# Optimization experiments

Hardware: AMD Instinct MI355X
Metric: run time of the kernel (lower is better)

The kernel has to match this reference:

```python
import jax, jax.numpy as jnp
import numpy as np

D_IN, D_OUT, SEQ, BATCH = 768, 768, 4096, 4

def setup_inputs() -> dict:
    key = jax.random.key(0)
    k0, k1, k2, k3 = jax.random.split(key, 4)
    s = 1.0 / np.sqrt(D_IN)
    return {
        "input_batch": jax.random.normal(k0, (BATCH, SEQ, D_IN), dtype=jnp.float32),
        "Wq": jax.random.uniform(k1, (D_OUT, D_IN), jnp.float32, -s, s),
        "Wk": jax.random.uniform(k2, (D_OUT, D_IN), jnp.float32, -s, s),
        "Wv": jax.random.uniform(k3, (D_OUT, D_IN), jnp.float32, -s, s),
    }

def reference(input_batch, Wq, Wk, Wv):
    B, N, d_in = input_batch.shape
    q = jnp.einsum('bnd,od->bno', input_batch, Wq)  # [B,N,d_out]
    k = jnp.einsum('bnd,od->bno', input_batch, Wk)
    v = jnp.einsum('bnd,od->bno', input_batch, Wv)
    scores = jnp.einsum('bqo,bko->bqk', q, k)  # [B,N,N]
    causal = jnp.tril(jnp.ones((N, N), dtype=bool))
    scores = jnp.where(causal, scores, -jnp.inf)
    # note: original scales by d_in (input embedding dim), not d_out
    weights = jax.nn.softmax(scores / jnp.sqrt(jnp.asarray(d_in, scores.dtype)), axis=-1)
    return jnp.einsum('bqk,bko->bqo', weights, v)
```

## Files before the change

kernel.cpp:

```cpp
#include <hip/hip_runtime.h>
#include <hip/hip_bf16.h>
#include <stdint.h>

#define NSEQ 4096
#define DDIM 768
#define NB   4
#define NTRI 528
#define BLKE 16384

typedef short short8 __attribute__((ext_vector_type(8)));
typedef float f32x16 __attribute__((ext_vector_type(16)));

__device__ __forceinline__ unsigned short f2bf(float f) {
    unsigned int u = __float_as_uint(f);
    u += 0x7fffu + ((u >> 16) & 1u);
    return (unsigned short)(u >> 16);
}
__device__ __forceinline__ float bf2f(unsigned short h) {
    return __uint_as_float(((unsigned int)h) << 16);
}
__device__ __forceinline__ short8 cvt8(const float* __restrict__ p) {
    float4 x = *(const float4*)p;
    float4 y = *(const float4*)(p + 4);
    union { short8 s; __hip_bfloat162 h[4]; } u;
    u.h[0] = __float22bfloat162_rn(make_float2(x.x, x.y));
    u.h[1] = __float22bfloat162_rn(make_float2(x.z, x.w));
    u.h[2] = __float22bfloat162_rn(make_float2(y.x, y.y));
    u.h[3] = __float22bfloat162_rn(make_float2(y.z, y.w));
    return u.s;
}

typedef const __attribute__((address_space(1))) unsigned int ga_u32;
typedef __attribute__((address_space(3))) unsigned int ls_u32;
__device__ __forceinline__ void gload_lds16(const void* g, void* l) {
    __builtin_amdgcn_global_load_lds((ga_u32*)(uintptr_t)g, (ls_u32*)(uintptr_t)l, 16, 0, 0);
}

__device__ __forceinline__ void stage_tile(const unsigned short* gbase, int stride,
                                           unsigned short* lds, int tid) {
    const int lane = tid & 63, wv = tid >> 6;
    const int r8  = lane >> 3;
    const int csw = ((lane & 7) ^ r8) * 8;
    const int cl  = (lane & 7) * 8;
#pragma unroll
    for (int t = 0; t < 4; ++t) {
        const int row = wv * 32 + t * 8 + r8;
        gload_lds16(gbase + (size_t)row * stride + csw, lds + row * 64 + cl);
    }
}

__device__ __forceinline__ void mma_tiles(const unsigned short* As, const unsigned short* Bs,
                                          f32x16 acc[2][2], int wm, int wn, int lane) {
    const int r32 = lane & 31;
    const int hi  = lane >> 5;
    const int sw  = lane & 7;
#pragma unroll
    for (int c = 0; c < 4; ++c) {
        const int chunk = ((c * 2 + hi) ^ sw) * 8;
        short8 af[2], bg[2];
#pragma unroll
        for (int mt = 0; mt < 2; ++mt)
            af[mt] = *(const short8*)(As + (wm * 64 + mt * 32 + r32) * 64 + chunk);
#pragma unroll
        for (int nt = 0; nt < 2; ++nt)
            bg[nt] = *(const short8*)(Bs + (wn * 64 + nt * 32 + r32) * 64 + chunk);
#pragma unroll
        for (int mt = 0; mt < 2; ++mt)
#pragma unroll
            for (int nt = 0; nt < 2; ++nt)
                acc[mt][nt] = __builtin_amdgcn_mfma_f32_32x32x16_bf16(af[mt], bg[nt], acc[mt][nt], 0, 0, 0);
    }
}

__device__ __forceinline__ int crow(int reg, int hi) {
    return (reg & 3) + 8 * (reg >> 2) + 4 * hi;
}

__global__ __launch_bounds__(256)
void convert_kernel(const float* __restrict__ X, const float* __restrict__ Wq,
                    const float* __restrict__ Wk, const float* __restrict__ Wv,
                    unsigned short* __restrict__ Xb, unsigned short* __restrict__ Wb,
                    unsigned int* __restrict__ counter)
{
    const int bid = blockIdx.x;
    if (bid == 0 && threadIdx.x == 0) *counter = 0u;
    const float* src; unsigned short* dst; size_t off;
    if (bid < 6144) { src = X; dst = Xb; off = (size_t)bid * 2048; }
    else {
        const int wbid = bid - 6144;
        const int wi = wbid / 288;
        src = (wi == 0) ? Wq : ((wi == 1) ? Wk : Wv);
        dst = Wb + (size_t)wi * (DDIM * DDIM);
        off = (size_t)(wbid - wi * 288) * 2048;
    }
    const size_t i = off + (size_t)threadIdx.x * 8;
    *(short8*)(dst + i) = cvt8(src + i);
}

__global__ __launch_bounds__(256)
void qkv_gemm(const unsigned short* __restrict__ Xb, const unsigned short* __restrict__ Wb,
              unsigned short* __restrict__ Qb, unsigned short* __restrict__ Kb,
              unsigned short* __restrict__ Vtb)
{
    const int tid = threadIdx.x, lane = tid & 63, wv = tid >> 6;
    const int r32 = lane & 31, hi = lane >> 5, wm = wv >> 1, wn = wv & 1;
    const int m0 = blockIdx.x * 128, n0 = blockIdx.y * 128, widx = blockIdx.z;
    const unsigned short* A = Xb + (size_t)m0 * DDIM;
    const unsigned short* B = Wb + (size_t)widx * (DDIM * DDIM) + (size_t)n0 * DDIM;

    __shared__ __align__(16) unsigned short As[128 * 64];
    __shared__ __align__(16) unsigned short Bs[128 * 64];

    f32x16 acc[2][2] = {};

    for (int kt = 0; kt < 12; ++kt) {
        stage_tile(A + kt * 64, DDIM, As, tid);
        stage_tile(B + kt * 64, DDIM, Bs, tid);
        __syncthreads();
        mma_tiles(As, Bs, acc, wm, wn, lane);
        __syncthreads();
    }

    const int m_base = m0 + wm * 64, o_base = n0 + wn * 64;
    if (widx < 2) {
        unsigned short* dst = (widx == 0) ? Qb : Kb;
#pragma unroll
        for (int mt = 0; mt < 2; ++mt)
#pragma unroll
            for (int nt = 0; nt < 2; ++nt)
#pragma unroll
                for (int reg = 0; reg < 16; ++reg)
                    dst[(size_t)(m_base + mt * 32 + crow(reg, hi)) * DDIM +
                        (o_base + nt * 32 + r32)] = f2bf(acc[mt][nt][reg]);
    } else {
        const int bb = m0 >> 12;
        const int n_seq0 = (m0 & (NSEQ - 1)) + wm * 64;
#pragma unroll
        for (int mt = 0; mt < 2; ++mt)
#pragma unroll
            for (int nt = 0; nt < 2; ++nt) {
                const int o = o_base + nt * 32 + r32;
#pragma unroll
                for (int b4 = 0; b4 < 4; ++b4) {
                    ushort4 pk;
                    pk.x = f2bf(acc[mt][nt][b4 * 4 + 0]);
                    pk.y = f2bf(acc[mt][nt][b4 * 4 + 1]);
                    pk.z = f2bf(acc[mt][nt][b4 * 4 + 2]);
                    pk.w = f2bf(acc[mt][nt][b4 * 4 + 3]);
                    const int n = n_seq0 + mt * 32 + b4 * 8 + hi * 4;
                    *(ushort4*)(Vtb + ((size_t)(bb * DDIM + o)) * NSEQ + n) = pk;
                }
            }
    }
}

__global__ __launch_bounds__(256)
void gemm_s(const unsigned short* __restrict__ Qb, const unsigned short* __restrict__ Kb,
            unsigned short* __restrict__ Sbuf)
{
    const int tid = threadIdx.x, lane = tid & 63, wv = tid >> 6;
    const int r32 = lane & 31, hi = lane >> 5, wm = wv >> 1, wn = wv & 1;
    const int idx = blockIdx.x, bb = blockIdx.y;
    int qb = (int)((sqrtf(8.f * idx + 1.f) - 1.f) * 0.5f);
    while ((qb + 1) * (qb + 2) / 2 <= idx) ++qb;
    while (qb * (qb + 1) / 2 > idx) --qb;
    const int kb = idx - qb * (qb + 1) / 2;

    const unsigned short* A = Qb + ((size_t)bb * NSEQ + qb * 128) * DDIM;
    const unsigned short* B = Kb + ((size_t)bb * NSEQ + kb * 128) * DDIM;

    __shared__ __align__(16) unsigned short As[128 * 64];
    __shared__ __align__(16) unsigned short Bs[128 * 64];

    f32x16 acc[2][2] = {};

    for (int kt = 0; kt < 12; ++kt) {
        stage_tile(A + kt * 64, DDIM, As, tid);
        stage_tile(B + kt * 64, DDIM, Bs, tid);
        __syncthreads();
        mma_tiles(As, Bs, acc, wm, wn, lane);
        __syncthreads();
    }

    unsigned short* Sblk = Sbuf + ((size_t)(bb * NTRI + idx)) * BLKE;
    const bool diag = (qb == kb);
#pragma unroll
    for (int mt = 0; mt < 2; ++mt)
#pragma unroll
        for (int nt = 0; nt < 2; ++nt)
#pragma unroll
            for (int reg = 0; reg < 16; ++reg) {
                const int row = wm * 64 + mt * 32 + crow(reg, hi);
                const int col = wn * 64 + nt * 32 + r32;
                unsigned short v = (diag && col > row) ? (unsigned short)0xFF80
                                                       : f2bf(acc[mt][nt][reg]);
                Sblk[row * 128 + col] = v;
            }
}

__global__ __launch_bounds__(256)
void softmax_kernel(unsigned short* __restrict__ S)
{
    const float c2 = 0.05205877475f;
    const int row = blockIdx.x * 4 + (threadIdx.x >> 6);
    const int lane = threadIdx.x & 63;
    const int bb = row >> 12, q = row & (NSEQ - 1);
    const int qb = q >> 7, ql = q & 127, nb = qb + 1;
    const size_t base = ((size_t)(bb * NTRI + qb * (qb + 1) / 2)) * BLKE + (size_t)ql * 128;
    const int g = lane >> 4, c = (lane & 15) * 8;

    const short NEGINF = (short)0xFF80;
    short8 regs[8];
#pragma unroll
    for (int it = 0; it < 8; ++it) {
        const int kb = it * 4 + g;
        if (kb < nb) {
            regs[it] = *(const short8*)(S + base + (size_t)kb * BLKE + c);
        } else {
            short8 v;
#pragma unroll
            for (int j = 0; j < 8; ++j) v[j] = NEGINF;
            regs[it] = v;
        }
    }

    float mx = -1e30f;
#pragma unroll
    for (int it = 0; it < 8; ++it)
#pragma unroll
        for (int j = 0; j < 8; ++j) mx = fmaxf(mx, bf2f((unsigned short)regs[it][j]));
#pragma unroll
    for (int s = 1; s < 64; s <<= 1) mx = fmaxf(mx, __shfl_xor(mx, s));

    float sum = 0.f;
#pragma unroll
    for (int it = 0; it < 8; ++it)
#pragma unroll
        for (int j = 0; j < 8; ++j)
            sum += exp2f((bf2f((unsigned short)regs[it][j]) - mx) * c2);
#pragma unroll
    for (int s = 1; s < 64; s <<= 1) sum += __shfl_xor(sum, s);
    const float inv = 1.0f / sum;

#pragma unroll
    for (int it = 0; it < 8; ++it) {
        const int kb = it * 4 + g;
        if (kb < nb) {
            short8 o;
#pragma unroll
            for (int j = 0; j < 8; ++j)
                o[j] = (short)f2bf(exp2f((bf2f((unsigned short)regs[it][j]) - mx) * c2) * inv);
            *(short8*)(S + base + (size_t)kb * BLKE + c) = o;
        }
    }
}

__global__ __launch_bounds__(256)
void gemm_pv(const unsigned short* __restrict__ P, const unsigned short* __restrict__ Vt,
             float* __restrict__ Out, unsigned int* __restrict__ counter)
{
    const int tid = threadIdx.x, lane = tid & 63, wv = tid >> 6;
    const int r32 = lane & 31, hi = lane >> 5, wm = wv >> 1, wn = wv & 1;

    __shared__ __align__(16) unsigned short As[128 * 64];
    __shared__ __align__(16) unsigned short Bs[128 * 64];
    __shared__ unsigned int item_s;

    for (;;) {
        if (tid == 0) item_s = atomicAdd(counter, 1u);
        __syncthreads();
        const unsigned int item = item_s;
        if (item >= 768u) return;

        const int t = (int)(item / 24u);
        const int qb = 31 - t;
        const int rem = (int)(item - (unsigned)t * 24u);
        const int bb = rem / 6, ob = rem % 6;
        const size_t triq = (size_t)qb * (qb + 1) / 2;
        const unsigned short* Pbat = P + (size_t)bb * NTRI * BLKE;
        const unsigned short* Bbase = Vt + ((size_t)(bb * DDIM + ob * 128)) * NSEQ;
        const int niter = (qb + 1) * 2;

        f32x16 acc[2][2] = {};

        for (int it = 0; it < niter; ++it) {
            const int k0 = it * 64;
            const int kblk = k0 >> 7, cb = k0 & 64;
            stage_tile(Pbat + (triq + kblk) * BLKE + cb, 128, As, tid);
            stage_tile(Bbase + k0, NSEQ, Bs, tid);
            __syncthreads();
            mma_tiles(As, Bs, acc, wm, wn, lane);
            __syncthreads();
        }

        const int q_base = qb * 128 + wm * 64;
        const int o_base = ob * 128 + wn * 64;
#pragma unroll
        for (int mt = 0; mt < 2; ++mt)
#pragma unroll
            for (int nt = 0; nt < 2; ++nt)
#pragma unroll
                for (int reg = 0; reg < 16; ++reg) {
                    const int q = q_base + mt * 32 + crow(reg, hi);
                    Out[((size_t)(bb * NSEQ + q)) * DDIM + (o_base + nt * 32 + r32)] =
                        acc[mt][nt][reg];
                }
    }
}

extern "C" void kernel_launch(void* const* d_in, const int* in_sizes, int n_in,
                              void* d_out, int out_size, void* d_ws, size_t ws_size,
                              hipStream_t stream)
{
    const float* X  = (const float*)d_in[0];
    const float* Wq = (const float*)d_in[1];
    const float* Wk = (const float*)d_in[2];
    const float* Wv = (const float*)d_in[3];
    float* Out = (float*)d_out;

    const size_t E = (size_t)NB * NSEQ * DDIM;
    char* ws = (char*)d_ws;
    unsigned short* Qb  = (unsigned short*)ws;
    unsigned short* Kb  = Qb + E;
    unsigned short* Vtb = Kb + E;
    unsigned short* Sbuf = Vtb + E;
    unsigned short* Xb  = Sbuf;
    unsigned short* Wb  = Xb + E;
    unsigned int* counter =
        (unsigned int*)(ws + 3 * E * 2 + (size_t)NB * NTRI * BLKE * 2);

    convert_kernel<<<7008, 256, 0, stream>>>(X, Wq, Wk, Wv, Xb, Wb, counter);
    qkv_gemm<<<dim3(128, 6, 3), 256, 0, stream>>>(Xb, Wb, Qb, Kb, Vtb);
    gemm_s<<<dim3(528, NB), 256, 0, stream>>>(Qb, Kb, Sbuf);
    softmax_kernel<<<4096, 256, 0, stream>>>(Sbuf);
    gemm_pv<<<512, 256, 0, stream>>>(Sbuf, Vtb, Out, counter);
}
```

Measured before the change: 381.4 us.

## Fuse softmax into score GEMM epilogue and defer normalization to PV GEMM

The separate softmax kernel is removed. The score GEMM epilogue now writes unnormalized exp2 values as bf16 and atomically accumulates per-row sums into a new L buffer, which the convert kernel zeroes. The PV GEMM scales each output row by the reciprocal of its row sum. This saves a full read and write pass over the score buffer and one kernel launch. The cost is a float atomic per row per block, and exponentials are taken without subtracting the row max, so large scores could overflow for inputs with a wider range than these.

```diff
diff --git a/kernel.cpp b/kernel.cpp
--- a/kernel.cpp
+++ b/kernel.cpp
@@ -80,10 +80,15 @@
 void convert_kernel(const float* __restrict__ X, const float* __restrict__ Wq,
                     const float* __restrict__ Wk, const float* __restrict__ Wv,
                     unsigned short* __restrict__ Xb, unsigned short* __restrict__ Wb,
-                    unsigned int* __restrict__ counter)
+                    float* __restrict__ L, unsigned int* __restrict__ counter)
 {
     const int bid = blockIdx.x;
     if (bid == 0 && threadIdx.x == 0) *counter = 0u;
+    if (bid >= 7008) {
+        const int idx = (bid - 7008) * 1024 + threadIdx.x * 4;
+        *(float4*)(L + idx) = make_float4(0.f, 0.f, 0.f, 0.f);
+        return;
+    }
     const float* src; unsigned short* dst; size_t off;
     if (bid < 6144) { src = X; dst = Xb; off = (size_t)bid * 2048; }
     else {
@@ -156,8 +161,9 @@
 
 __global__ __launch_bounds__(256)
 void gemm_s(const unsigned short* __restrict__ Qb, const unsigned short* __restrict__ Kb,
-            unsigned short* __restrict__ Sbuf)
-{
+            unsigned short* __restrict__ Sbuf, float* __restrict__ L)
+{
+    const float c2 = 0.05205877475f;
     const int tid = threadIdx.x, lane = tid & 63, wv = tid >> 6;
     const int r32 = lane & 31, hi = lane >> 5, wm = wv >> 1, wn = wv & 1;
     const int idx = blockIdx.x, bb = blockIdx.y;
@@ -183,87 +189,42 @@
     }
 
     unsigned short* Sblk = Sbuf + ((size_t)(bb * NTRI + idx)) * BLKE;
+    float* Lrow = L + (size_t)bb * NSEQ + qb * 128;
     const bool diag = (qb == kb);
 #pragma unroll
     for (int mt = 0; mt < 2; ++mt)
 #pragma unroll
-        for (int nt = 0; nt < 2; ++nt)
-#pragma unroll
-            for (int reg = 0; reg < 16; ++reg) {
-                const int row = wm * 64 + mt * 32 + crow(reg, hi);
+        for (int reg = 0; reg < 16; ++reg) {
+            const int row = wm * 64 + mt * 32 + crow(reg, hi);
+            float vsum = 0.f;
+#pragma unroll
+            for (int nt = 0; nt < 2; ++nt) {
                 const int col = wn * 64 + nt * 32 + r32;
-                unsigned short v = (diag && col > row) ? (unsigned short)0xFF80
-                                                       : f2bf(acc[mt][nt][reg]);
-                Sblk[row * 128 + col] = v;
+                float e = (diag && col > row) ? 0.f : exp2f(acc[mt][nt][reg] * c2);
+                const unsigned short pb = f2bf(e);
+                Sblk[row * 128 + col] = pb;
+                vsum += bf2f(pb);
             }
-}
-
-__global__ __launch_bounds__(256)
-void softmax_kernel(unsigned short* __restrict__ S)
-{
-    const float c2 = 0.05205877475f;
-    const int row = blockIdx.x * 4 + (threadIdx.x >> 6);
-    const int lane = threadIdx.x & 63;
-    const int bb = row >> 12, q = row & (NSEQ - 1);
-    const int qb = q >> 7, ql = q & 127, nb = qb + 1;
-    const size_t base = ((size_t)(bb * NTRI + qb * (qb + 1) / 2)) * BLKE + (size_t)ql * 128;
-    const int g = lane >> 4, c = (lane & 15) * 8;
-
-    const short NEGINF = (short)0xFF80;
-    short8 regs[8];
-#pragma unroll
-    for (int it = 0; it < 8; ++it) {
-        const int kb = it * 4 + g;
-        if (kb < nb) {
-            regs[it] = *(const short8*)(S + base + (size_t)kb * BLKE + c);
-        } else {
-            short8 v;
-#pragma unroll
-            for (int j = 0; j < 8; ++j) v[j] = NEGINF;
-            regs[it] = v;
+            vsum += __shfl_xor(vsum, 1);
+            vsum += __shfl_xor(vsum, 2);
+            vsum += __shfl_xor(vsum, 4);
+            vsum += __shfl_xor(vsum, 8);
+            vsum += __shfl_xor(vsum, 16);
+            if (r32 == 0) atomicAdd(&Lrow[row], vsum);
         }
-    }
-
-    float mx = -1e30f;
-#pragma unroll
-    for (int it = 0; it < 8; ++it)
-#pragma unroll
-        for (int j = 0; j < 8; ++j) mx = fmaxf(mx, bf2f((unsigned short)regs[it][j]));
-#pragma unroll
-    for (int s = 1; s < 64; s <<= 1) mx = fmaxf(mx, __shfl_xor(mx, s));
-
-    float sum = 0.f;
-#pragma unroll
-    for (int it = 0; it < 8; ++it)
-#pragma unroll
-        for (int j = 0; j < 8; ++j)
-            sum += exp2f((bf2f((unsigned short)regs[it][j]) - mx) * c2);
-#pragma unroll
-    for (int s = 1; s < 64; s <<= 1) sum += __shfl_xor(sum, s);
-    const float inv = 1.0f / sum;
-
-#pragma unroll
-    for (int it = 0; it < 8; ++it) {
-        const int kb = it * 4 + g;
-        if (kb < nb) {
-            short8 o;
-#pragma unroll
-            for (int j = 0; j < 8; ++j)
-                o[j] = (short)f2bf(exp2f((bf2f((unsigned short)regs[it][j]) - mx) * c2) * inv);
-            *(short8*)(S + base + (size_t)kb * BLKE + c) = o;
-        }
-    }
 }
 
 __global__ __launch_bounds__(256)
 void gemm_pv(const unsigned short* __restrict__ P, const unsigned short* __restrict__ Vt,
-             float* __restrict__ Out, unsigned int* __restrict__ counter)
+             const float* __restrict__ L, float* __restrict__ Out,
+             unsigned int* __restrict__ counter)
 {
     const int tid = threadIdx.x, lane = tid & 63, wv = tid >> 6;
     const int r32 = lane & 31, hi = lane >> 5, wm = wv >> 1, wn = wv & 1;
 
     __shared__ __align__(16) unsigned short As[128 * 64];
     __shared__ __align__(16) unsigned short Bs[128 * 64];
+    __shared__ float Linv[128];
     __shared__ unsigned int item_s;
 
     for (;;) {
@@ -280,6 +241,8 @@
         const unsigned short* Pbat = P + (size_t)bb * NTRI * BLKE;
         const unsigned short* Bbase = Vt + ((size_t)(bb * DDIM + ob * 128)) * NSEQ;
         const int niter = (qb + 1) * 2;
+
+        if (tid < 128) Linv[tid] = 1.0f / L[(size_t)bb * NSEQ + qb * 128 + tid];
 
         f32x16 acc[2][2] = {};
 
@@ -301,9 +264,10 @@
             for (int nt = 0; nt < 2; ++nt)
 #pragma unroll
                 for (int reg = 0; reg < 16; ++reg) {
-                    const int q = q_base + mt * 32 + crow(reg, hi);
+                    const int rl = wm * 64 + mt * 32 + crow(reg, hi);
+                    const int q = qb * 128 + rl;
                     Out[((size_t)(bb * NSEQ + q)) * DDIM + (o_base + nt * 32 + r32)] =
-                        acc[mt][nt][reg];
+                        acc[mt][nt][reg] * Linv[rl];
                 }
     }
 }
@@ -326,12 +290,11 @@
     unsigned short* Sbuf = Vtb + E;
     unsigned short* Xb  = Sbuf;
     unsigned short* Wb  = Xb + E;
-    unsigned int* counter =
-        (unsigned int*)(ws + 3 * E * 2 + (size_t)NB * NTRI * BLKE * 2);
-
-    convert_kernel<<<7008, 256, 0, stream>>>(X, Wq, Wk, Wv, Xb, Wb, counter);
+    float* L = (float*)(ws + 3 * E * 2 + (size_t)NB * NTRI * BLKE * 2);
+    unsigned int* counter = (unsigned int*)(L + (size_t)NB * NSEQ);
+
+    convert_kernel<<<7024, 256, 0, stream>>>(X, Wq, Wk, Wv, Xb, Wb, L, counter);
     qkv_gemm<<<dim3(128, 6, 3), 256, 0, stream>>>(Xb, Wb, Qb, Kb, Vtb);
-    gemm_s<<<dim3(528, NB), 256, 0, stream>>>(Qb, Kb, Sbuf);
-    softmax_kernel<<<4096, 256, 0, stream>>>(Sbuf);
-    gemm_pv<<<512, 256, 0, stream>>>(Sbuf, Vtb, Out, counter);
-}
+    gemm_s<<<dim3(528, NB), 256, 0, stream>>>(Qb, Kb, Sbuf, L);
+    gemm_pv<<<512, 256, 0, stream>>>(Sbuf, Vtb, L, Out, counter);
+}
```

Result: faster. 373.7 us (-2.0%).
